# Kernel optimization log

Measured on AMD Instinct MI355X. Metric: run time of the kernel, lower is better.

## Reference

```python
import jax, jax.numpy as jnp
import numpy as np

N = 50000      # nodes
E = 800000     # edges (avg degree 16)
IN = 256       # input feature dim
HID = 128      # hidden dim
H = 4          # heads
C = HID // H   # per-head dim = 32
L = 3          # layers


def setup_inputs() -> dict:
    key = jax.random.key(0)
    ks = jax.random.split(key, 16)
    s = 0.02
    f32 = jnp.float32
    inp = {
        "x": jax.random.normal(ks[0], (N, IN), f32),
        "edge_index": jax.random.randint(ks[1], (2, E), 0, N, dtype=jnp.int32),
        "edge_attr": jax.random.normal(ks[2], (E, 1), f32),
        "Wi": jax.random.normal(ks[3], (IN, HID), f32) * s,
        "bi": jnp.zeros((HID,), f32),
        "Wq": jax.random.normal(ks[4], (L, HID, HID), f32) * s,
        "bq": jnp.zeros((L, HID), f32),
        "Wk": jax.random.normal(ks[5], (L, HID, HID), f32) * s,
        "bk": jnp.zeros((L, HID), f32),
        "Wv": jax.random.normal(ks[6], (L, HID, HID), f32) * s,
        "bv": jnp.zeros((L, HID), f32),
        "We": jax.random.normal(ks[7], (L, 1, HID), f32) * s,      # lin_edge, no bias
        "Wskip": jax.random.normal(ks[8], (L, HID, HID), f32) * s,
        "bskip": jnp.zeros((L, HID), f32),
        "Wbeta": jax.random.normal(ks[9], (L, 3 * HID, 1), f32) * s,  # lin_beta, no bias
        "ln_g": jnp.ones((L, HID), f32),
        "ln_b": jnp.zeros((L, HID), f32),
    }
    return inp


def _layer_norm(x, g, b, eps=1e-5):
    mu = jnp.mean(x, axis=-1, keepdims=True)
    var = jnp.var(x, axis=-1, keepdims=True)
    return (x - mu) * jax.lax.rsqrt(var + eps) * g + b


def _transformer_conv(h, src, dst, edge_attr, Wq, bq, Wk, bk, Wv, bv, We, Wskip, bskip, Wbeta):
    # node-level projections [N, HID]
    q = h @ Wq + bq
    k = h @ Wk + bk
    v = h @ Wv + bv
    e = edge_attr @ We                       # [E, HID] edge embedding
    # per-edge gathered features [E, H, C]
    qi = q[dst].reshape(E, H, C)
    kj = (k[src] + e).reshape(E, H, C)
    vj = (v[src] + e).reshape(E, H, C)
    # attention logits [E, H]
    alpha = jnp.sum(qi * kj, axis=-1) / np.sqrt(C)
    # segment softmax over destination node
    amax = jax.ops.segment_max(alpha, dst, num_segments=N)   # [N, H]
    ex = jnp.exp(alpha - amax[dst])
    denom = jax.ops.segment_sum(ex, dst, num_segments=N)     # [N, H]
    attn = ex / (denom[dst] + 1e-16)                         # [E, H]
    # scatter-add aggregation -> [N, H, C] -> concat heads [N, HID]
    out = jax.ops.segment_sum(attn[..., None] * vj, dst, num_segments=N).reshape(N, HID)
    # gated skip (beta=True, root_weight=True)
    x_r = h @ Wskip + bskip
    beta = jax.nn.sigmoid(jnp.concatenate([out, x_r, out - x_r], axis=-1) @ Wbeta)  # [N, 1]
    return beta * x_r + (1.0 - beta) * out


def reference(x, edge_index, edge_attr, Wi, bi, Wq, bq, Wk, bk, Wv, bv, We, Wskip, bskip, Wbeta, ln_g, ln_b):
    src = edge_index[0]
    dst = edge_index[1]
    h = x @ Wi + bi
    for l in range(L):
        res = h
        h = _transformer_conv(h, src, dst, edge_attr,
                              Wq[l], bq[l], Wk[l], bk[l], Wv[l], bv[l],
                              We[l], Wskip[l], bskip[l], Wbeta[l])
        h = jax.nn.gelu(h, approximate=False)
        h = _layer_norm(h + res, ln_g[l], ln_b[l])
        # dropout: eval mode -> identity
    return h
```

## Files before the change

### kernel.cpp

```cpp
#include <hip/hip_runtime.h>
#include <math.h>

#define NNODES 50000
#define NEDGES 800000
#define DIN 256
#define DHID 128
#define GBLK 391
#define NBUCK 196
#define CHUNK 4096

typedef __attribute__((ext_vector_type(8))) short short8;
typedef __attribute__((ext_vector_type(4))) float f32x4;
typedef __attribute__((ext_vector_type(2))) float f32x2;

__device__ __forceinline__ unsigned short f2bf(float f) {
    unsigned u = __builtin_bit_cast(unsigned, f);
    u += 0x7fffu + ((u >> 16) & 1u);
    return (unsigned short)(u >> 16);
}
__device__ __forceinline__ float bf2f(unsigned short s) {
    return __builtin_bit_cast(float, (unsigned)s << 16);
}
__device__ __forceinline__ unsigned packbf(float a, float b) {
    return (unsigned)f2bf(a) | ((unsigned)f2bf(b) << 16);
}
__device__ __forceinline__ float dpp_xor1(float x) {
    return __builtin_bit_cast(float, __builtin_amdgcn_update_dpp(0, __builtin_bit_cast(int, x), 0xB1, 0xF, 0xF, true));
}
__device__ __forceinline__ float dpp_xor2(float x) {
    return __builtin_bit_cast(float, __builtin_amdgcn_update_dpp(0, __builtin_bit_cast(int, x), 0x4E, 0xF, 0xF, true));
}
__device__ __forceinline__ float dpp_hmirror(float x) {
    return __builtin_bit_cast(float, __builtin_amdgcn_update_dpp(0, __builtin_bit_cast(int, x), 0x141, 0xF, 0xF, true));
}
__device__ __forceinline__ float dpp_mirror(float x) {
    return __builtin_bit_cast(float, __builtin_amdgcn_update_dpp(0, __builtin_bit_cast(int, x), 0x140, 0xF, 0xF, true));
}
__device__ __forceinline__ float red16(float x) {
    x += dpp_xor1(x);
    x += dpp_xor2(x);
    x += dpp_hmirror(x);
    x += dpp_mirror(x);
    return x;
}

__global__ __launch_bounds__(256) void prep_hist(const float* __restrict__ Wi, const float* __restrict__ Wq,
                                                 const float* __restrict__ Wk, const float* __restrict__ Wv,
                                                 const float* __restrict__ Ws, unsigned short* __restrict__ Wit,
                                                 unsigned short* __restrict__ Wt3, const int* __restrict__ dst,
                                                 int* __restrict__ counts, int pb) {
    if ((int)blockIdx.x < pb) {
        int idx = blockIdx.x * 256 + threadIdx.x;
        if (idx < DHID * DIN) {
            int n = idx >> 8, kk = idx & 255;
            Wit[idx] = f2bf(Wi[kk * DHID + n]);
        }
        int idx2 = idx - DHID * DIN;
        if (idx2 >= 0 && idx2 < 3 * 512 * DHID) {
            int l = idx2 / (512 * DHID);
            int rem = idx2 - l * 512 * DHID;
            int r = rem >> 7;
            int kk = rem & 127;
            int sel = r >> 7, rl = r & 127;
            const float* srcm = sel == 0 ? Wq : sel == 1 ? Wk : sel == 2 ? Wv : Ws;
            Wt3[idx2] = f2bf(srcm[l * DHID * DHID + kk * DHID + rl]);
        }
    } else {
        int e = (blockIdx.x - pb) * 256 + threadIdx.x;
        if (e < NEDGES) atomicAdd(&counts[dst[e]], 1);
    }
}

__global__ __launch_bounds__(256) void k_scan_block(const int* __restrict__ in, int* __restrict__ out,
                                                    int* __restrict__ partials, int n) {
    __shared__ int sh[256];
    int tid = threadIdx.x;
    int i = blockIdx.x * 256 + tid;
    int vv = (i < n) ? in[i] : 0;
    sh[tid] = vv;
    __syncthreads();
    for (int off = 1; off < 256; off <<= 1) {
        int t = (tid >= off) ? sh[tid - off] : 0;
        __syncthreads();
        sh[tid] += t;
        __syncthreads();
    }
    if (i < n) out[i] = sh[tid];
    if (tid == 255) partials[blockIdx.x] = sh[255];
}

__global__ __launch_bounds__(256) void k_apply2(const int* __restrict__ partials, int* __restrict__ row_ptr, int n,
                                                int nb) {
    __shared__ int sh[256];
    int tid = threadIdx.x;
    int vv = (tid < nb) ? partials[tid] : 0;
    sh[tid] = vv;
    __syncthreads();
    for (int off = 1; off < 256; off <<= 1) {
        int t = (tid >= off) ? sh[tid - off] : 0;
        __syncthreads();
        sh[tid] += t;
        __syncthreads();
    }
    int i = blockIdx.x * 256 + tid;
    if (i < n) {
        int add = blockIdx.x ? sh[blockIdx.x - 1] : 0;
        row_ptr[i + 1] += add;
    }
    if (i == 0) row_ptr[0] = 0;
}

__global__ __launch_bounds__(256) void bin_edges(const int* __restrict__ src, const int* __restrict__ dst,
                                                 const float* __restrict__ ea, const int* __restrict__ row_ptr,
                                                 int* __restrict__ bfill, unsigned* __restrict__ brec,
                                                 unsigned char* __restrict__ bdst) {
    __shared__ int hist[NBUCK];
    __shared__ int lbase[NBUCK];
    __shared__ int gbase[NBUCK];
    __shared__ int cnt[NBUCK];
    __shared__ unsigned rec4[CHUNK];
    __shared__ unsigned char dl8[CHUNK];
    __shared__ unsigned char bk8[CHUNK];
    const int tid = threadIdx.x;
    const int e0 = blockIdx.x * CHUNK;
    const int n = min(NEDGES - e0, CHUNK);
    for (int i = tid; i < NBUCK; i += 256) hist[i] = 0;
    __syncthreads();
    for (int i = tid; i < n; i += 256) atomicAdd(&hist[dst[e0 + i] >> 8], 1);
    __syncthreads();
    if (tid == 0) {
        int run = 0;
        for (int b = 0; b < NBUCK; ++b) {
            lbase[b] = run;
            run += hist[b];
        }
    }
    __syncthreads();
    for (int b = tid; b < NBUCK; b += 256) {
        int h = hist[b];
        int off = h ? atomicAdd(&bfill[b], h) : 0;
        gbase[b] = row_ptr[b << 8] + off;
        cnt[b] = lbase[b];
    }
    __syncthreads();
    for (int i = tid; i < n; i += 256) {
        int d = dst[e0 + i];
        int b = d >> 8;
        int lp = atomicAdd(&cnt[b], 1);
        rec4[lp] = (unsigned)src[e0 + i] | ((unsigned)f2bf(ea[e0 + i]) << 16);
        dl8[lp] = (unsigned char)(d & 255);
        bk8[lp] = (unsigned char)b;
    }
    __syncthreads();
    for (int i = tid; i < n; i += 256) {
        int b = bk8[i];
        int pos = gbase[b] + (i - lbase[b]);
        brec[pos] = rec4[i];
        bdst[pos] = dl8[i];
    }
}

__global__ __launch_bounds__(256) void sort_bucket(const unsigned* __restrict__ brec,
                                                   const unsigned char* __restrict__ bdst,
                                                   const int* __restrict__ row_ptr, unsigned* __restrict__ esrc) {
    __shared__ int rp[257];
    __shared__ int cnt[256];
    const int b = blockIdx.x;
    const int d0 = b << 8;
    const int nmax = min(256, NNODES - d0);
    const int tid = threadIdx.x;
    for (int i = tid; i <= nmax; i += 256) rp[i] = row_ptr[d0 + i];
    cnt[tid] = 0;
    __syncthreads();
    const int base = rp[0], end = rp[nmax];
    for (int i = base + tid; i < end; i += 256) {
        unsigned rec = brec[i];
        int d = bdst[i];
        int rank = atomicAdd(&cnt[d], 1);
        esrc[rp[d] + rank] = rec;
    }
}

__global__ __launch_bounds__(256) void gemm_in(const float* __restrict__ A, const unsigned short* __restrict__ Wt,
                                               const float* __restrict__ bias, unsigned* __restrict__ h32, int M) {
    __shared__ short As[128 * 128];
    const int tid = threadIdx.x;
    const int lane = tid & 63;
    const int wid = tid >> 6;
    const int row0 = blockIdx.x * 128;
    const int wr = (wid & 1) * 64;
    const int wc = (wid >> 1) * 64;
    f32x4 acc[4][4] = {};
    const int srow = tid >> 1;
    const int sk = (tid & 1) * 64;
    const int grow = min(row0 + srow, M - 1);
    for (int kt = 0; kt < 2; ++kt) {
        const float* ap = A + (size_t)grow * DIN + kt * 128 + sk;
#pragma unroll
        for (int i = 0; i < 8; ++i) {
            float4 f0 = *(const float4*)(ap + i * 8);
            float4 f1 = *(const float4*)(ap + i * 8 + 4);
            short8 s;
            s[0] = f2bf(f0.x); s[1] = f2bf(f0.y); s[2] = f2bf(f0.z); s[3] = f2bf(f0.w);
            s[4] = f2bf(f1.x); s[5] = f2bf(f1.y); s[6] = f2bf(f1.z); s[7] = f2bf(f1.w);
            int g = (sk >> 3) + i;
            *(short8*)(&As[srow * 128 + ((g ^ (srow & 7)) << 3)]) = s;
        }
        __syncthreads();
#pragma unroll
        for (int ks = 0; ks < 4; ++ks) {
            short8 a[4], b[4];
#pragma unroll
            for (int m = 0; m < 4; ++m) {
                int r = wr + m * 16 + (lane & 15);
                int g = ks * 4 + (lane >> 4);
                a[m] = *(const short8*)(&As[r * 128 + ((g ^ (r & 7)) << 3)]);
            }
#pragma unroll
            for (int n = 0; n < 4; ++n) {
                int c = wc + n * 16 + (lane & 15);
                b[n] = *(const short8*)(Wt + (size_t)c * DIN + kt * 128 + ks * 32 + (lane >> 4) * 8);
            }
#pragma unroll
            for (int m = 0; m < 4; ++m)
#pragma unroll
                for (int n = 0; n < 4; ++n)
                    acc[m][n] = __builtin_amdgcn_mfma_f32_16x16x32_bf16(a[m], b[n], acc[m][n], 0, 0, 0);
        }
        __syncthreads();
    }
    float* my = ((float*)As) + wid * 1024;
    float bb[4];
#pragma unroll
    for (int n = 0; n < 4; ++n) bb[n] = bias[wc + n * 16 + (lane & 15)];
    const int rr = lane >> 2;
    const int cb = lane & 3;
#pragma unroll
    for (int m = 0; m < 4; ++m) {
#pragma unroll
        for (int n = 0; n < 4; ++n) {
            int lc = n * 16 + (lane & 15);
#pragma unroll
            for (int j = 0; j < 4; ++j) {
                int row = (lane >> 4) * 4 + j;
                my[row * 64 + (((lc >> 2) ^ (row & 7)) << 2) + (lc & 3)] = acc[m][n][j] + bb[n];
            }
        }
        float vals[16];
#pragma unroll
        for (int s = 0; s < 4; ++s) {
            int gx = (cb * 4 + s) ^ (rr & 7);
            f32x4 t4 = *(const f32x4*)(my + rr * 64 + gx * 4);
            vals[s * 4 + 0] = t4.x; vals[s * 4 + 1] = t4.y; vals[s * 4 + 2] = t4.z; vals[s * 4 + 3] = t4.w;
        }
        int grow2 = row0 + wr + m * 16 + rr;
        if (grow2 < M) {
            unsigned pk[8];
#pragma unroll
            for (int d = 0; d < 8; ++d) pk[d] = packbf(vals[2 * d], vals[2 * d + 1]);
            unsigned* op = h32 + (size_t)grow2 * 64 + (wc >> 1) + cb * 8;
            *(uint4*)op = make_uint4(pk[0], pk[1], pk[2], pk[3]);
            *(uint4*)(op + 4) = make_uint4(pk[4], pk[5], pk[6], pk[7]);
        }
    }
}

__global__ __launch_bounds__(512) void gemm_qkvs(const unsigned short* __restrict__ A,
                                                 const unsigned short* __restrict__ Wt, const float* __restrict__ bq,
                                                 const float* __restrict__ bk, const float* __restrict__ bv,
                                                 const float* __restrict__ bs, unsigned* __restrict__ q32,
                                                 unsigned* __restrict__ kv, unsigned* __restrict__ xr32, int M) {
    __shared__ short As[128 * 128];
    const int tid = threadIdx.x;
    const int lane = tid & 63;
    const int wid = tid >> 6;
    const int row0 = blockIdx.x * 128;
    const int sel = wid >> 2;
    const int wr = (wid & 1) * 64;
    const int wc = ((wid >> 1) & 1) * 64;
    f32x4 acc0[4][4] = {}, acc1[4][4] = {};
    {
        const int srow = tid >> 2;
        const int sk = (tid & 3) * 32;
        const int grow = min(row0 + srow, M - 1);
        const unsigned short* ap = A + (size_t)grow * DHID + sk;
#pragma unroll
        for (int i = 0; i < 4; ++i) {
            short8 s = *(const short8*)(ap + i * 8);
            int g = (sk >> 3) + i;
            *(short8*)(&As[srow * 128 + ((g ^ (srow & 7)) << 3)]) = s;
        }
    }
    __syncthreads();
    const int b0base = sel ? 128 : 0;
    const int b1base = sel ? 256 : 384;
#pragma unroll
    for (int ks = 0; ks < 4; ++ks) {
        short8 a[4], b0[4], b1[4];
#pragma unroll
        for (int m = 0; m < 4; ++m) {
            int r = wr + m * 16 + (lane & 15);
            int g = ks * 4 + (lane >> 4);
            a[m] = *(const short8*)(&As[r * 128 + ((g ^ (r & 7)) << 3)]);
        }
#pragma unroll
        for (int n = 0; n < 4; ++n) {
            int rb = wc + n * 16 + (lane & 15);
            b0[n] = *(const short8*)(Wt + (size_t)(b0base + rb) * DHID + ks * 32 + (lane >> 4) * 8);
            b1[n] = *(const short8*)(Wt + (size_t)(b1base + rb) * DHID + ks * 32 + (lane >> 4) * 8);
        }
#pragma unroll
        for (int m = 0; m < 4; ++m)
#pragma unroll
            for (int n = 0; n < 4; ++n) {
                acc0[m][n] = __builtin_amdgcn_mfma_f32_16x16x32_bf16(a[m], b0[n], acc0[m][n], 0, 0, 0);
                acc1[m][n] = __builtin_amdgcn_mfma_f32_16x16x32_bf16(a[m], b1[n], acc1[m][n], 0, 0, 0);
            }
    }
    __syncthreads();
    float* my = ((float*)As) + wid * 1024;
    const float* bias0 = sel ? bk : bq;
    const float* bias1 = sel ? bv : bs;
    float bb0[4], bb1[4];
#pragma unroll
    for (int n = 0; n < 4; ++n) {
        int c = wc + n * 16 + (lane & 15);
        bb0[n] = bias0[c];
        bb1[n] = bias1[c];
    }
    const int rr = lane >> 2;
    const int cb = lane & 3;
#pragma unroll
    for (int m = 0; m < 4; ++m) {
        float vals0[16], vals1[16];
#pragma unroll
        for (int n = 0; n < 4; ++n) {
            int lc = n * 16 + (lane & 15);
#pragma unroll
            for (int j = 0; j < 4; ++j) {
                int row = (lane >> 4) * 4 + j;
                my[row * 64 + (((lc >> 2) ^ (row & 7)) << 2) + (lc & 3)] = acc0[m][n][j] + bb0[n];
            }
        }
#pragma unroll
        for (int s = 0; s < 4; ++s) {
            int gx = (cb * 4 + s) ^ (rr & 7);
            f32x4 t4 = *(const f32x4*)(my + rr * 64 + gx * 4);
            vals0[s * 4 + 0] = t4.x; vals0[s * 4 + 1] = t4.y; vals0[s * 4 + 2] = t4.z; vals0[s * 4 + 3] = t4.w;
        }
#pragma unroll
        for (int n = 0; n < 4; ++n) {
            int lc = n * 16 + (lane & 15);
#pragma unroll
            for (int j = 0; j < 4; ++j) {
                int row = (lane >> 4) * 4 + j;
                my[row * 64 + (((lc >> 2) ^ (row & 7)) << 2) + (lc & 3)] = acc1[m][n][j] + bb1[n];
            }
        }
#pragma unroll
        for (int s = 0; s < 4; ++s) {
            int gx = (cb * 4 + s) ^ (rr & 7);
            f32x4 t4 = *(const f32x4*)(my + rr * 64 + gx * 4);
            vals1[s * 4 + 0] = t4.x; vals1[s * 4 + 1] = t4.y; vals1[s * 4 + 2] = t4.z; vals1[s * 4 + 3] = t4.w;
        }
        int grow2 = row0 + wr + m * 16 + rr;
        if (grow2 < M) {
            size_t obase = (size_t)grow2 * 64 + (wc >> 1) + cb * 8;
            if (sel == 0) {
                unsigned p0[8], p1[8];
#pragma unroll
                for (int d = 0; d < 8; ++d) {
                    p0[d] = packbf(vals0[2 * d], vals0[2 * d + 1]);
                    p1[d] = packbf(vals1[2 * d], vals1[2 * d + 1]);
                }
                *(uint4*)(q32 + obase) = make_uint4(p0[0], p0[1], p0[2], p0[3]);
                *(uint4*)(q32 + obase + 4) = make_uint4(p0[4], p0[5], p0[6], p0[7]);
                *(uint4*)(xr32 + obase) = make_uint4(p1[0], p1[1], p1[2], p1[3]);
                *(uint4*)(xr32 + obase + 4) = make_uint4(p1[4], p1[5], p1[6], p1[7]);
            } else {
                unsigned pk[8];
#pragma unroll
                for (int d = 0; d < 8; ++d) {
                    unsigned u = (unsigned)__builtin_amdgcn_cvt_pk_fp8_f32(vals0[2 * d], vals0[2 * d + 1], 0, false);
                    u = (unsigned)__builtin_amdgcn_cvt_pk_fp8_f32(vals1[2 * d], vals1[2 * d + 1], (int)u, true);
                    pk[d] = u;
                }
                *(uint4*)(kv + obase) = make_uint4(pk[0], pk[1], pk[2], pk[3]);
                *(uint4*)(kv + obase + 4) = make_uint4(pk[4], pk[5], pk[6], pk[7]);
            }
        }
    }
}

__global__ __launch_bounds__(256) void node_attn_fuse(const unsigned* __restrict__ q32,
                                                      const unsigned* __restrict__ kv, const unsigned* __restrict__ esrc,
                                                      const float* __restrict__ We, const int* __restrict__ row_ptr,
                                                      const unsigned* __restrict__ xr32, const unsigned* res32,
                                                      const float* __restrict__ Wb, const float* __restrict__ lng,
                                                      const float* __restrict__ lnb, unsigned* houtb, float* houtf) {
    const int tid = threadIdx.x;
    const int lane = tid & 63;
    const int lnl = lane & 15;
    const int gbase = lane & 48;
    const int node = blockIdx.x * 16 + (tid >> 4);
    const int base = row_ptr[node], end = row_ptr[node + 1];
    const float SC = 0.25505654047688565f;
    const float THR = 8.0f;

    float qv[8], wev[8];
    {
        uint4 qw = *(const uint4*)(q32 + (size_t)node * 64 + 4 * lnl);
        unsigned qd[4] = {qw.x, qw.y, qw.z, qw.w};
#pragma unroll
        for (int t = 0; t < 4; ++t) {
            qv[2 * t] = bf2f((unsigned short)qd[t]) * SC;
            qv[2 * t + 1] = bf2f((unsigned short)(qd[t] >> 16)) * SC;
        }
        float4 wlo = *(const float4*)(We + 8 * lnl);
        float4 whi = *(const float4*)(We + 8 * lnl + 4);
        wev[0] = wlo.x; wev[1] = wlo.y; wev[2] = wlo.z; wev[3] = wlo.w;
        wev[4] = whi.x; wev[5] = whi.y; wev[6] = whi.z; wev[7] = whi.w;
    }
    float qwe;
    {
        float s = 0.f;
#pragma unroll
        for (int i = 0; i < 8; ++i) s = fmaf(qv[i], wev[i], s);
        s += dpp_xor1(s);
        s += dpp_xor2(s);
        qwe = s;
    }

    float m = -1e30f, sden = 0.f, tacc = 0.f;
    float acc[8] = {};
    const unsigned* kvp = kv + 4 * lnl;

    for (int off = 0; ; off += 16) {
        int cnt = min(end - base - off, 16);
        if (__all(cnt <= 0)) break;
        unsigned u_l = 0;
        if (lnl < cnt) u_l = esrc[base + off + lnl];
        int cm = max(cnt, 0);
        cm = max(cm, __shfl_xor(cm, 16));
        cm = max(cm, __shfl_xor(cm, 32));
        unsigned ue0 = (unsigned)__shfl((int)u_l, gbase + 0);
        unsigned ue1 = (unsigned)__shfl((int)u_l, gbase + 1);
        uint4 kw0 = *(const uint4*)(kvp + (size_t)(ue0 & 0xFFFFu) * 64);
        uint4 kw1 = *(const uint4*)(kvp + (size_t)(ue1 & 0xFFFFu) * 64);
        for (int j = 0; j < cm; j += 2) {
            uint4 ka = kw0, kb = kw1;
            unsigned ua = ue0, ub = ue1;
            if (j + 2 < cm) {
                ue0 = (unsigned)__shfl((int)u_l, gbase + j + 2);
                ue1 = (unsigned)__shfl((int)u_l, gbase + j + 3);
                kw0 = *(const uint4*)(kvp + (size_t)(ue0 & 0xFFFFu) * 64);
                kw1 = *(const uint4*)(kvp + (size_t)(ue1 & 0xFFFFu) * 64);
            }
            float av0 = bf2f((unsigned short)(ua >> 16));
            float av1 = bf2f((unsigned short)(ub >> 16));
            unsigned kd0[4] = {ka.x, ka.y, ka.z, ka.w};
            unsigned kd1[4] = {kb.x, kb.y, kb.z, kb.w};
            float vj0[8], vj1[8];
            float p0 = 0.f, p1 = 0.f;
#pragma unroll
            for (int t = 0; t < 4; ++t) {
                f32x2 k0 = __builtin_amdgcn_cvt_pk_f32_fp8((int)kd0[t], false);
                f32x2 v0 = __builtin_amdgcn_cvt_pk_f32_fp8((int)kd0[t], true);
                f32x2 k1 = __builtin_amdgcn_cvt_pk_f32_fp8((int)kd1[t], false);
                f32x2 v1 = __builtin_amdgcn_cvt_pk_f32_fp8((int)kd1[t], true);
                p0 = fmaf(qv[2 * t], k0.x, p0);
                p0 = fmaf(qv[2 * t + 1], k0.y, p0);
                p1 = fmaf(qv[2 * t], k1.x, p1);
                p1 = fmaf(qv[2 * t + 1], k1.y, p1);
                vj0[2 * t] = v0.x; vj0[2 * t + 1] = v0.y;
                vj1[2 * t] = v1.x; vj1[2 * t + 1] = v1.y;
            }
            p0 += dpp_xor1(p0);
            p0 += dpp_xor2(p0);
            p1 += dpp_xor1(p1);
            p1 += dpp_xor2(p1);
            p0 = fmaf(av0, qwe, p0);
            p1 = fmaf(av1, qwe, p1);
            p0 = (j < cnt) ? p0 : -3e38f;
            p1 = (j + 1 < cnt) ? p1 : -3e38f;
            float pm = fmaxf(p0, p1);
            if (__any(pm - m > THR)) {
                float mn2 = fmaxf(m, pm);
                float sc = exp2f(m - mn2);
                float w0 = exp2f(p0 - mn2), w1 = exp2f(p1 - mn2);
                sden = fmaf(sden, sc, w0 + w1);
                tacc = fmaf(tacc, sc, fmaf(w0, av0, w1 * av1));
#pragma unroll
                for (int i = 0; i < 8; ++i) acc[i] = fmaf(acc[i], sc, fmaf(w0, vj0[i], w1 * vj1[i]));
                m = mn2;
            } else {
                float w0 = exp2f(p0 - m), w1 = exp2f(p1 - m);
                sden += w0 + w1;
                tacc = fmaf(w0, av0, fmaf(w1, av1, tacc));
#pragma unroll
                for (int i = 0; i < 8; ++i) acc[i] = fmaf(w0, vj0[i], fmaf(w1, vj1[i], acc[i]));
            }
        }
    }

    float rden = 1.f / (sden + 1e-16f);
    float o[8];
#pragma unroll
    for (int i = 0; i < 8; ++i) o[i] = fmaf(tacc, wev[i], acc[i]) * rden;

    float x[8];
    {
        uint4 xw = *(const uint4*)(xr32 + (size_t)node * 64 + 4 * lnl);
        unsigned xd[4] = {xw.x, xw.y, xw.z, xw.w};
#pragma unroll
        for (int t = 0; t < 4; ++t) {
            x[2 * t] = bf2f((unsigned short)xd[t]);
            x[2 * t + 1] = bf2f((unsigned short)(xd[t] >> 16));
        }
    }
    float bl = 0.f;
#pragma unroll
    for (int t = 0; t < 2; ++t) {
        float4 w0 = *(const float4*)(Wb + 8 * lnl + 4 * t);
        float4 w1 = *(const float4*)(Wb + 128 + 8 * lnl + 4 * t);
        float4 w2 = *(const float4*)(Wb + 256 + 8 * lnl + 4 * t);
        bl = fmaf(o[4 * t], w0.x, bl); bl = fmaf(o[4 * t + 1], w0.y, bl);
        bl = fmaf(o[4 * t + 2], w0.z, bl); bl = fmaf(o[4 * t + 3], w0.w, bl);
        bl = fmaf(x[4 * t], w1.x, bl); bl = fmaf(x[4 * t + 1], w1.y, bl);
        bl = fmaf(x[4 * t + 2], w1.z, bl); bl = fmaf(x[4 * t + 3], w1.w, bl);
        bl = fmaf(o[4 * t] - x[4 * t], w2.x, bl); bl = fmaf(o[4 * t + 1] - x[4 * t + 1], w2.y, bl);
        bl = fmaf(o[4 * t + 2] - x[4 * t + 2], w2.z, bl); bl = fmaf(o[4 * t + 3] - x[4 * t + 3], w2.w, bl);
    }
    bl = red16(bl);
    float beta = 1.f / (1.f + __expf(-bl));
    float tpre[8];
    {
        uint4 rw = *(const uint4*)(res32 + (size_t)node * 64 + 4 * lnl);
        unsigned rd[4] = {rw.x, rw.y, rw.z, rw.w};
#pragma unroll
        for (int i = 0; i < 8; ++i) {
            float gg = beta * x[i] + (1.f - beta) * o[i];
            gg = 0.5f * gg * (1.f + erff(gg * 0.70710678118654752f));
            float rv = (i & 1) ? bf2f((unsigned short)(rd[i >> 1] >> 16)) : bf2f((unsigned short)rd[i >> 1]);
            tpre[i] = gg + rv;
        }
    }
    float su = 0.f, sq = 0.f;
#pragma unroll
    for (int i = 0; i < 8; ++i) {
        su += tpre[i];
        sq = fmaf(tpre[i], tpre[i], sq);
    }
    su = red16(su);
    sq = red16(sq);
    float mu = su * (1.f / 128.f);
    float var = sq * (1.f / 128.f) - mu * mu;
    float inv = rsqrtf(var + 1e-5f);
    float4 g0 = *(const float4*)(lng + 8 * lnl);
    float4 g1 = *(const float4*)(lng + 8 * lnl + 4);
    float4 b0 = *(const float4*)(lnb + 8 * lnl);
    float4 b1 = *(const float4*)(lnb + 8 * lnl + 4);
    float gg[8] = {g0.x, g0.y, g0.z, g0.w, g1.x, g1.y, g1.z, g1.w};
    float bb[8] = {b0.x, b0.y, b0.z, b0.w, b1.x, b1.y, b1.z, b1.w};
    float ov[8];
#pragma unroll
    for (int i = 0; i < 8; ++i) ov[i] = (tpre[i] - mu) * inv * gg[i] + bb[i];
    if (houtf) {
        float* op = houtf + (size_t)node * 128 + 8 * lnl;
        *(float4*)op = make_float4(ov[0], ov[1], ov[2], ov[3]);
        *(float4*)(op + 4) = make_float4(ov[4], ov[5], ov[6], ov[7]);
    } else {
        unsigned pk[4];
#pragma unroll
        for (int d = 0; d < 4; ++d) pk[d] = packbf(ov[2 * d], ov[2 * d + 1]);
        *(uint4*)(houtb + (size_t)node * 64 + 4 * lnl) = make_uint4(pk[0], pk[1], pk[2], pk[3]);
    }
}

extern "C" void kernel_launch(void* const* d_in, const int* in_sizes, int n_in, void* d_out, int out_size,
                              void* d_ws, size_t ws_size, hipStream_t stream) {
    const float* x = (const float*)d_in[0];
    const int* ei = (const int*)d_in[1];
    const float* ea = (const float*)d_in[2];
    const float* Wi = (const float*)d_in[3];
    const float* bi = (const float*)d_in[4];
    const float* Wq = (const float*)d_in[5];
    const float* bq = (const float*)d_in[6];
    const float* Wk = (const float*)d_in[7];
    const float* bk = (const float*)d_in[8];
    const float* Wv = (const float*)d_in[9];
    const float* bv = (const float*)d_in[10];
    const float* We = (const float*)d_in[11];
    const float* Wskip = (const float*)d_in[12];
    const float* bskip = (const float*)d_in[13];
    const float* Wbeta = (const float*)d_in[14];
    const float* lng = (const float*)d_in[15];
    const float* lnb = (const float*)d_in[16];

    const int* srcp = ei;
    const int* dstp = ei + NEDGES;

    char* p = (char*)d_ws;
    auto alloc = [&](size_t bytes) {
        void* r = (void*)p;
        p += (bytes + 255) & ~(size_t)255;
        return r;
    };
    unsigned* h32 = (unsigned*)alloc((size_t)NNODES * 64 * 4);
    unsigned* q32 = (unsigned*)alloc((size_t)NNODES * 64 * 4);
    unsigned* xr32 = (unsigned*)alloc((size_t)NNODES * 64 * 4);
    unsigned* kv = (unsigned*)alloc((size_t)NNODES * 64 * 4);
    unsigned short* Wit = (unsigned short*)alloc((size_t)DHID * DIN * 2);
    unsigned short* Wt3 = (unsigned short*)alloc((size_t)3 * 512 * DHID * 2);
    int* counts = (int*)alloc((size_t)(NNODES + 256) * 4);
    int* bfill = counts + NNODES;
    int* row_ptr = (int*)alloc((size_t)(NNODES + 1) * 4);
    unsigned* esrc = (unsigned*)alloc((size_t)NEDGES * 4);
    unsigned* brec = (unsigned*)alloc((size_t)NEDGES * 4);
    unsigned char* bdst = (unsigned char*)alloc((size_t)NEDGES);
    int* partials = (int*)alloc(256 * 4);

    const int EB = (NEDGES + 255) / 256;
    const int NB = (NNODES + 255) / 256;
    const int WB = NNODES / 16;
    const int PB = (DHID * DIN + 3 * 512 * DHID + 255) / 256;
    const int AB = (NEDGES + CHUNK - 1) / CHUNK;

    hipMemsetAsync(counts, 0, (size_t)(NNODES + 256) * 4, stream);
    prep_hist<<<PB + EB, 256, 0, stream>>>(Wi, Wq, Wk, Wv, Wskip, Wit, Wt3, dstp, counts, PB);
    gemm_in<<<GBLK, 256, 0, stream>>>(x, Wit, bi, h32, NNODES);
    k_scan_block<<<NB, 256, 0, stream>>>(counts, row_ptr + 1, partials, NNODES);
    k_apply2<<<NB, 256, 0, stream>>>(partials, row_ptr, NNODES, NB);
    bin_edges<<<AB, 256, 0, stream>>>(srcp, dstp, ea, row_ptr, bfill, brec, bdst);
    sort_bucket<<<NBUCK, 256, 0, stream>>>(brec, bdst, row_ptr, esrc);

    for (int l = 0; l < 3; ++l) {
        const size_t bo = (size_t)l * 128;
        gemm_qkvs<<<GBLK, 512, 0, stream>>>((const unsigned short*)h32, Wt3 + (size_t)l * 512 * DHID, bq + bo, bk + bo,
                                            bv + bo, bskip + bo, q32, kv, xr32, NNODES);
        node_attn_fuse<<<WB, 256, 0, stream>>>(q32, kv, esrc, We + bo, row_ptr, xr32, h32,
                                               Wbeta + (size_t)l * 384, lng + bo, lnb + bo, h32,
                                               (l == 2) ? (float*)d_out : nullptr);
    }
}
```

Before: 312.7 us.

## Sort nodes by degree for attention, deepen gather prefetch, shrink QKV GEMM tiles

```diff
diff --git a/kernel.cpp b/kernel.cpp
--- a/kernel.cpp
+++ b/kernel.cpp
@@ -6,6 +6,7 @@
 #define DIN 256
 #define DHID 128
 #define GBLK 391
+#define QBLK 782
 #define NBUCK 196
 #define CHUNK 4096
 
@@ -72,13 +73,16 @@
 }
 
 __global__ __launch_bounds__(256) void k_scan_block(const int* __restrict__ in, int* __restrict__ out,
-                                                    int* __restrict__ partials, int n) {
+                                                    int* __restrict__ partials, int n, int* __restrict__ dh) {
     __shared__ int sh[256];
+    __shared__ int dhist[256];
     int tid = threadIdx.x;
     int i = blockIdx.x * 256 + tid;
     int vv = (i < n) ? in[i] : 0;
     sh[tid] = vv;
-    __syncthreads();
+    dhist[tid] = 0;
+    __syncthreads();
+    if (i < n) atomicAdd(&dhist[min(vv, 255)], 1);
     for (int off = 1; off < 256; off <<= 1) {
         int t = (tid >= off) ? sh[tid - off] : 0;
         __syncthreads();
@@ -87,10 +91,13 @@
     }
     if (i < n) out[i] = sh[tid];
     if (tid == 255) partials[blockIdx.x] = sh[255];
+    __syncthreads();
+    int hc = dhist[tid];
+    if (hc) atomicAdd(&dh[tid], hc);
 }
 
 __global__ __launch_bounds__(256) void k_apply2(const int* __restrict__ partials, int* __restrict__ row_ptr, int n,
-                                                int nb) {
+                                                int nb, const int* __restrict__ dh, int* __restrict__ dbase) {
     __shared__ int sh[256];
     int tid = threadIdx.x;
     int vv = (tid < nb) ? partials[tid] : 0;
@@ -108,6 +115,39 @@
         row_ptr[i + 1] += add;
     }
     if (i == 0) row_ptr[0] = 0;
+    if (blockIdx.x == 0) {
+        __syncthreads();
+        int c = dh[255 - tid];
+        sh[tid] = c;
+        __syncthreads();
+        for (int off = 1; off < 256; off <<= 1) {
+            int t = (tid >= off) ? sh[tid - off] : 0;
+            __syncthreads();
+            sh[tid] += t;
+            __syncthreads();
+        }
+        dbase[255 - tid] = sh[tid] - c;
+    }
+}
+
+__global__ __launch_bounds__(256) void perm_scatter(const int* __restrict__ counts, const int* __restrict__ dbase,
+                                                    int* __restrict__ dfill, int* __restrict__ perm) {
+    __shared__ int h[256], gb[256], c2[256];
+    const int tid = threadIdx.x;
+    int i = blockIdx.x * 256 + tid;
+    int d = (i < NNODES) ? min(counts[i], 255) : -1;
+    h[tid] = 0;
+    c2[tid] = 0;
+    __syncthreads();
+    if (d >= 0) atomicAdd(&h[d], 1);
+    __syncthreads();
+    int c = h[tid];
+    gb[tid] = c ? dbase[tid] + atomicAdd(&dfill[tid], c) : 0;
+    __syncthreads();
+    if (d >= 0) {
+        int r = atomicAdd(&c2[d], 1);
+        perm[gb[d] + r] = i;
+    }
 }
 
 __global__ __launch_bounds__(256) void bin_edges(const int* __restrict__ src, const int* __restrict__ dst,
@@ -265,19 +305,18 @@
     }
 }
 
-__global__ __launch_bounds__(512) void gemm_qkvs(const unsigned short* __restrict__ A,
+__global__ __launch_bounds__(256) void gemm_qkvs(const unsigned short* __restrict__ A,
                                                  const unsigned short* __restrict__ Wt, const float* __restrict__ bq,
                                                  const float* __restrict__ bk, const float* __restrict__ bv,
                                                  const float* __restrict__ bs, unsigned* __restrict__ q32,
                                                  unsigned* __restrict__ kv, unsigned* __restrict__ xr32, int M) {
-    __shared__ short As[128 * 128];
+    __shared__ short As[64 * 128];
     const int tid = threadIdx.x;
     const int lane = tid & 63;
     const int wid = tid >> 6;
-    const int row0 = blockIdx.x * 128;
-    const int sel = wid >> 2;
-    const int wr = (wid & 1) * 64;
-    const int wc = ((wid >> 1) & 1) * 64;
+    const int row0 = blockIdx.x * 64;
+    const int sel = wid >> 1;
+    const int wc = (wid & 1) * 64;
     f32x4 acc0[4][4] = {}, acc1[4][4] = {};
     {
         const int srow = tid >> 2;
@@ -299,7 +338,7 @@
         short8 a[4], b0[4], b1[4];
 #pragma unroll
         for (int m = 0; m < 4; ++m) {
-            int r = wr + m * 16 + (lane & 15);
+            int r = m * 16 + (lane & 15);
             int g = ks * 4 + (lane >> 4);
             a[m] = *(const short8*)(&As[r * 128 + ((g ^ (r & 7)) << 3)]);
         }
@@ -363,7 +402,7 @@
             f32x4 t4 = *(const f32x4*)(my + rr * 64 + gx * 4);
             vals1[s * 4 + 0] = t4.x; vals1[s * 4 + 1] = t4.y; vals1[s * 4 + 2] = t4.z; vals1[s * 4 + 3] = t4.w;
         }
-        int grow2 = row0 + wr + m * 16 + rr;
+        int grow2 = row0 + m * 16 + rr;
         if (grow2 < M) {
             size_t obase = (size_t)grow2 * 64 + (wc >> 1) + cb * 8;
             if (sel == 0) {
@@ -395,14 +434,15 @@
 __global__ __launch_bounds__(256) void node_attn_fuse(const unsigned* __restrict__ q32,
                                                       const unsigned* __restrict__ kv, const unsigned* __restrict__ esrc,
                                                       const float* __restrict__ We, const int* __restrict__ row_ptr,
-                                                      const unsigned* __restrict__ xr32, const unsigned* res32,
-                                                      const float* __restrict__ Wb, const float* __restrict__ lng,
-                                                      const float* __restrict__ lnb, unsigned* houtb, float* houtf) {
+                                                      const int* __restrict__ perm, const unsigned* __restrict__ xr32,
+                                                      const unsigned* res32, const float* __restrict__ Wb,
+                                                      const float* __restrict__ lng, const float* __restrict__ lnb,
+                                                      unsigned* houtb, float* houtf) {
     const int tid = threadIdx.x;
     const int lane = tid & 63;
     const int lnl = lane & 15;
     const int gbase = lane & 48;
-    const int node = blockIdx.x * 16 + (tid >> 4);
+    const int node = perm[blockIdx.x * 16 + (tid >> 4)];
     const int base = row_ptr[node], end = row_ptr[node + 1];
     const float SC = 0.25505654047688565f;
     const float THR = 8.0f;
@@ -445,16 +485,21 @@
         cm = max(cm, __shfl_xor(cm, 32));
         unsigned ue0 = (unsigned)__shfl((int)u_l, gbase + 0);
         unsigned ue1 = (unsigned)__shfl((int)u_l, gbase + 1);
+        unsigned ue2 = (unsigned)__shfl((int)u_l, gbase + 2);
+        unsigned ue3 = (unsigned)__shfl((int)u_l, gbase + 3);
         uint4 kw0 = *(const uint4*)(kvp + (size_t)(ue0 & 0xFFFFu) * 64);
         uint4 kw1 = *(const uint4*)(kvp + (size_t)(ue1 & 0xFFFFu) * 64);
+        uint4 kw2 = *(const uint4*)(kvp + (size_t)(ue2 & 0xFFFFu) * 64);
+        uint4 kw3 = *(const uint4*)(kvp + (size_t)(ue3 & 0xFFFFu) * 64);
         for (int j = 0; j < cm; j += 2) {
             uint4 ka = kw0, kb = kw1;
             unsigned ua = ue0, ub = ue1;
-            if (j + 2 < cm) {
-                ue0 = (unsigned)__shfl((int)u_l, gbase + j + 2);
-                ue1 = (unsigned)__shfl((int)u_l, gbase + j + 3);
-                kw0 = *(const uint4*)(kvp + (size_t)(ue0 & 0xFFFFu) * 64);
-                kw1 = *(const uint4*)(kvp + (size_t)(ue1 & 0xFFFFu) * 64);
+            ue0 = ue2; ue1 = ue3; kw0 = kw2; kw1 = kw3;
+            if (j + 4 < cm) {
+                ue2 = (unsigned)__shfl((int)u_l, gbase + j + 4);
+                ue3 = (unsigned)__shfl((int)u_l, gbase + j + 5);
+                kw2 = *(const uint4*)(kvp + (size_t)(ue2 & 0xFFFFu) * 64);
+                kw3 = *(const uint4*)(kvp + (size_t)(ue3 & 0xFFFFu) * 64);
             }
             float av0 = bf2f((unsigned short)(ua >> 16));
             float av1 = bf2f((unsigned short)(ub >> 16));
@@ -612,8 +657,12 @@
     unsigned* kv = (unsigned*)alloc((size_t)NNODES * 64 * 4);
     unsigned short* Wit = (unsigned short*)alloc((size_t)DHID * DIN * 2);
     unsigned short* Wt3 = (unsigned short*)alloc((size_t)3 * 512 * DHID * 2);
-    int* counts = (int*)alloc((size_t)(NNODES + 256) * 4);
+    int* counts = (int*)alloc((size_t)(NNODES + 768) * 4);
     int* bfill = counts + NNODES;
+    int* dh = bfill + 256;
+    int* dfill = dh + 256;
+    int* dbase = (int*)alloc(256 * 4);
+    int* perm = (int*)alloc((size_t)NNODES * 4);
     int* row_ptr = (int*)alloc((size_t)(NNODES + 1) * 4);
     unsigned* esrc = (unsigned*)alloc((size_t)NEDGES * 4);
     unsigned* brec = (unsigned*)alloc((size_t)NEDGES * 4);
@@ -626,19 +675,20 @@
     const int PB = (DHID * DIN + 3 * 512 * DHID + 255) / 256;
     const int AB = (NEDGES + CHUNK - 1) / CHUNK;
 
-    hipMemsetAsync(counts, 0, (size_t)(NNODES + 256) * 4, stream);
+    hipMemsetAsync(counts, 0, (size_t)(NNODES + 768) * 4, stream);
     prep_hist<<<PB + EB, 256, 0, stream>>>(Wi, Wq, Wk, Wv, Wskip, Wit, Wt3, dstp, counts, PB);
     gemm_in<<<GBLK, 256, 0, stream>>>(x, Wit, bi, h32, NNODES);
-    k_scan_block<<<NB, 256, 0, stream>>>(counts, row_ptr + 1, partials, NNODES);
-    k_apply2<<<NB, 256, 0, stream>>>(partials, row_ptr, NNODES, NB);
+    k_scan_block<<<NB, 256, 0, stream>>>(counts, row_ptr + 1, partials, NNODES, dh);
+    k_apply2<<<NB, 256, 0, stream>>>(partials, row_ptr, NNODES, NB, dh, dbase);
+    perm_scatter<<<NB, 256, 0, stream>>>(counts, dbase, dfill, perm);
     bin_edges<<<AB, 256, 0, stream>>>(srcp, dstp, ea, row_ptr, bfill, brec, bdst);
     sort_bucket<<<NBUCK, 256, 0, stream>>>(brec, bdst, row_ptr, esrc);
 
     for (int l = 0; l < 3; ++l) {
         const size_t bo = (size_t)l * 128;
-        gemm_qkvs<<<GBLK, 512, 0, stream>>>((const unsigned short*)h32, Wt3 + (size_t)l * 512 * DHID, bq + bo, bk + bo,
+        gemm_qkvs<<<QBLK, 256, 0, stream>>>((const unsigned short*)h32, Wt3 + (size_t)l * 512 * DHID, bq + bo, bk + bo,
                                             bv + bo, bskip + bo, q32, kv, xr32, NNODES);
-        node_attn_fuse<<<WB, 256, 0, stream>>>(q32, kv, esrc, We + bo, row_ptr, xr32, h32,
+        node_attn_fuse<<<WB, 256, 0, stream>>>(q32, kv, esrc, We + bo, row_ptr, perm, xr32, h32,
                                                Wbeta + (size_t)l * 384, lng + bo, lnb + bo, h32,
                                                (l == 2) ? (float*)d_out : nullptr);
     }
```

After: 324.2 us, median of 2. 1.04x slower.
